# Optimization experiments

Hardware: AMD Instinct MI355X
Metric: run time of the kernel (lower is better)

The kernel has to match this reference:

```python
import jax, jax.numpy as jnp
import numpy as np

B, D_IN, D_EXP, D_TOW, N_EXP, N_TASK = 16384, 1024, 1024, 512, 8, 4


def setup_inputs() -> dict:
    key = jax.random.key(0)
    ks = jax.random.split(key, 8)
    s_in = 1.0 / np.sqrt(D_IN)
    s_exp = 1.0 / np.sqrt(D_EXP)
    s_tow = 1.0 / np.sqrt(D_TOW)
    return {
        "x": jax.random.normal(ks[0], (B, D_IN), jnp.float32),
        # gate: ParameterList of num_experts vectors of size input_size -> [D_IN, N_EXP] matrix
        "gate_w": jax.random.normal(ks[1], (D_IN, N_EXP), jnp.float32) * s_in,
        # per-expert SLP: Linear(input_size, expert_size) + ReLU
        "exp_w": jax.random.normal(ks[2], (N_EXP, D_IN, D_EXP), jnp.float32) * s_in,
        "exp_b": jax.random.normal(ks[3], (N_EXP, D_EXP), jnp.float32) * 0.01,
        # per-task tower MLP: Linear(expert_size, tower_size) + ReLU + Linear(tower_size, 1)
        "tw1": jax.random.normal(ks[4], (N_TASK, D_EXP, D_TOW), jnp.float32) * s_exp,
        "tb1": jax.random.normal(ks[5], (N_TASK, D_TOW), jnp.float32) * 0.01,
        "tw2": jax.random.normal(ks[6], (N_TASK, D_TOW, 1), jnp.float32) * s_tow,
        "tb2": jax.random.normal(ks[7], (N_TASK, 1), jnp.float32) * 0.01,
    }


def reference(x, gate_w, exp_w, exp_b, tw1, tb1, tw2, tb2):
    # gates = x @ gate (no softmax in original)        [B, E]
    gates = x @ gate_w
    # all experts in one batched GEMM                  [E, B, D_exp]
    h = jax.nn.relu(jnp.einsum("bi,eid->ebd", x, exp_w) + exp_b[:, None, :])
    # fused gate-weighted combine (replaces the nested Python loops)
    shared = jnp.einsum("be,ebd->bd", gates, h)        # [B, D_exp]
    # per-task towers, batched over tasks
    t = jax.nn.relu(jnp.einsum("bd,tdh->tbh", shared, tw1) + tb1[:, None, :])
    outs = jnp.einsum("tbh,tho->tbo", t, tw2) + tb2[:, None, :]  # [T, B, 1]
    return outs
```

## Files before the change

### kernel.cpp

```cpp
#include <hip/hip_runtime.h>
#include <hip/hip_bf16.h>

#define B_DIM   16384
#define D_IN    1024
#define D_EXP   1024
#define D_TOW   512
#define N_EXPT  8
#define N_TASK  4

typedef _Float16 f16x8 __attribute__((ext_vector_type(8)));
typedef _Float16 f16x4 __attribute__((ext_vector_type(4)));
typedef float    f32x4 __attribute__((ext_vector_type(4)));

__device__ __forceinline__ void gll16(const void* g, void* l) {
  __builtin_amdgcn_global_load_lds(
      (const __attribute__((address_space(1))) unsigned int*)g,
      (__attribute__((address_space(3))) unsigned int*)l,
      16, 0, 0);
}

__device__ __forceinline__ f16x8 ldfrag(const _Float16* sM, int rowbase, int ks, int lane) {
  int rl = rowbase + (lane & 15);
  int ch = ((ks << 2) + (lane >> 4)) ^ (rl & 7);
  return *(const f16x8*)&sM[rl * 64 + ch * 8];
}

__global__ __launch_bounds__(256) void prep_x_kernel(
    const float* __restrict__ x, const float* __restrict__ gw,
    _Float16* __restrict__ xh, float* __restrict__ gates)
{
  __shared__ float sred[4][8];
  const int t = threadIdx.x;
  const long row = blockIdx.x;
  float4 v = ((const float4*)(x + row * D_IN))[t];
  f16x4 h;
  h[0] = (_Float16)v.x; h[1] = (_Float16)v.y; h[2] = (_Float16)v.z; h[3] = (_Float16)v.w;
  ((f16x4*)(xh + row * D_IN))[t] = h;

  float g[8];
#pragma unroll
  for (int e = 0; e < 8; ++e) g[e] = 0.f;
  const float* wp = gw + (size_t)t * 4 * 8;
  float xs[4] = {v.x, v.y, v.z, v.w};
#pragma unroll
  for (int j = 0; j < 4; ++j)
#pragma unroll
    for (int e = 0; e < 8; ++e) g[e] += xs[j] * wp[j * 8 + e];

#pragma unroll
  for (int e = 0; e < 8; ++e) {
    g[e] += __shfl_xor(g[e], 1);  g[e] += __shfl_xor(g[e], 2);
    g[e] += __shfl_xor(g[e], 4);  g[e] += __shfl_xor(g[e], 8);
    g[e] += __shfl_xor(g[e], 16); g[e] += __shfl_xor(g[e], 32);
  }
  if ((t & 63) == 0) {
#pragma unroll
    for (int e = 0; e < 8; ++e) sred[t >> 6][e] = g[e];
  }
  __syncthreads();
  if (t < 8) gates[row * 8 + t] = sred[0][t] + sred[1][t] + sred[2][t] + sred[3][t];
}

__global__ __launch_bounds__(256) void transpose_cvt_kernel(
    const float* __restrict__ in, _Float16* __restrict__ outp, int K, int N)
{
  __shared__ float tile[64][65];
  const int t = threadIdx.x;
  const int tx = t & 63, ty = t >> 6;
  const int n0 = blockIdx.x * 64;
  const int k0 = blockIdx.y * 64;
  const long s = blockIdx.z;
  const float* ip = in + s * (long)K * N;
  _Float16* op = outp + s * (long)K * N;
#pragma unroll
  for (int i = 0; i < 16; ++i) {
    int r = ty * 16 + i;
    tile[r][tx] = ip[(long)(k0 + r) * N + n0 + tx];
  }
  __syncthreads();
#pragma unroll
  for (int i = 0; i < 16; ++i) {
    int r = ty * 16 + i;
    op[(long)(n0 + r) * K + k0 + tx] = (_Float16)tile[tx][r];
  }
}

__global__ void init_out_kernel(float* __restrict__ out, const float* __restrict__ tb2) {
  int i = blockIdx.x * 256 + threadIdx.x;
  if (i < N_TASK * B_DIM) out[i] = tb2[i >> 14];
}

#define PHASE(SLOT, H, STAGES, WAITS)                                          \
  do {                                                                         \
    const _Float16* sAq = &sT[SLOT][(wm >> 1) * 8192];                         \
    const _Float16* sBq = &sT[SLOT][16384 + wn * 4096];                        \
    f16x8 af[2][2];                                                            \
    _Pragma("unroll") for (int m2 = 0; m2 < 2; ++m2)                           \
      _Pragma("unroll") for (int ks = 0; ks < 2; ++ks)                         \
        af[m2][ks] = ldfrag(sAq, (wm & 1) * 64 + ((H) * 2 + m2) * 16, ks, lane);\
    if ((H) == 0) {                                                            \
      _Pragma("unroll") for (int nf = 0; nf < 4; ++nf)                         \
        _Pragma("unroll") for (int ks = 0; ks < 2; ++ks)                       \
          bf[nf][ks] = ldfrag(sBq, nf * 16, ks, lane);                         \
    }                                                                          \
    STAGES;                                                                    \
    asm volatile("" ::: "memory");                                             \
    __builtin_amdgcn_s_barrier();                                              \
    asm volatile("s_waitcnt lgkmcnt(0)" ::: "memory");                         \
    __builtin_amdgcn_sched_barrier(0);                                         \
    __builtin_amdgcn_s_setprio(1);                                             \
    _Pragma("unroll") for (int m2 = 0; m2 < 2; ++m2)                           \
      _Pragma("unroll") for (int nf = 0; nf < 4; ++nf)                         \
        _Pragma("unroll") for (int ks = 0; ks < 2; ++ks)                       \
          acc[(H) * 2 + m2][nf] = __builtin_amdgcn_mfma_f32_16x16x32_f16(      \
              af[m2][ks], bf[nf][ks], acc[(H) * 2 + m2][nf], 0, 0, 0);         \
    __builtin_amdgcn_s_setprio(0);                                             \
    WAITS;                                                                     \
    asm volatile("" ::: "memory");                                             \
    __builtin_amdgcn_s_barrier();                                              \
  } while (0)

__global__ __launch_bounds__(512, 2) void moe_expert_kernel(
    const _Float16* __restrict__ xh,
    const _Float16* __restrict__ ewT,
    const float* __restrict__ expb,
    const float* __restrict__ gates,
    _Float16* __restrict__ shout)
{
  __shared__ alignas(16) _Float16 sT[2][24576];
  __shared__ float sG[256 * 8];
  __shared__ float sBias[8 * 128];
  const int t = threadIdx.x;
  const int lane = t & 63;
  const int wave = t >> 6;
  const int wm = wave >> 1, wn = wave & 1;
  const long row0 = (long)blockIdx.x * 256;
  const int col0 = blockIdx.y * 128;

  for (int i = t; i < 256 * 8; i += 512) sG[i] = gates[row0 * 8 + i];
  for (int i = t; i < 8 * 128; i += 512)
    sBias[i] = expb[(i >> 7) * D_EXP + col0 + (i & 127)];

  const int so_t = (((t & 7) ^ ((t >> 3) & 7)) << 4);
  const char* aBase = (const char*)xh + row0 * 2048 + (size_t)(t >> 3) * 2048 + so_t;
  const char* bRoot = (const char*)ewT + (size_t)col0 * 2048 + (size_t)(t >> 3) * 2048 + so_t;

  auto SA = [&](int s, int h, int step) {
    const char* g = aBase + (size_t)h * 262144 + (size_t)(step & 15) * 128;
    char* d = (char*)&sT[s][h * 8192] + t * 16;
    gll16(g, d);
    gll16(g + 131072, d + 8192);
    asm volatile("" ::: "memory");
  };
  auto SB = [&](int s, int h, int step) {
    const char* g = bRoot + (size_t)(step >> 4) * 2097152 + (size_t)h * 131072
                    + (size_t)(step & 15) * 128;
    char* d = (char*)&sT[s][16384 + h * 4096] + t * 16;
    gll16(g, d);
    asm volatile("" ::: "memory");
  };

  __syncthreads();

  SB(0, 0, 0); SB(0, 1, 0);
  SA(0, 0, 0); SA(0, 1, 0);
  SB(1, 0, 1); SB(1, 1, 1);
  asm volatile("s_waitcnt vmcnt(2)" ::: "memory");
  __builtin_amdgcn_s_barrier();

  f32x4 acc[4][4] = {};
  f32x4 shacc[4][4] = {};
  f16x8 bf[4][2];

  for (int it = 0; it < 64; ++it) {
    const int kt1 = 2 * it + 1;
    const bool pf = (it < 63);

    PHASE(0, 0, { SA(1, 0, kt1); SA(1, 1, kt1); }, {});
    PHASE(0, 1, { if (pf) { SB(0, 0, 2 * it + 2); SB(0, 1, 2 * it + 2); } },
          { if (pf) { asm volatile("s_waitcnt vmcnt(2)" ::: "memory"); }
            else    { asm volatile("s_waitcnt vmcnt(0)" ::: "memory"); } });
    PHASE(1, 0, { if (pf) { SA(0, 0, 2 * it + 2); SA(0, 1, 2 * it + 2); } }, {});
    PHASE(1, 1, { if (pf) { SB(1, 0, 2 * it + 3); SB(1, 1, 2 * it + 3); } },
          { if (pf) { asm volatile("s_waitcnt vmcnt(2)" ::: "memory"); } });

    if ((it & 7) == 7) {
      const int e = it >> 3;
      float bias4[4];
#pragma unroll
      for (int nf = 0; nf < 4; ++nf)
        bias4[nf] = sBias[e * 128 + wn * 64 + nf * 16 + (lane & 15)];
#pragma unroll
      for (int mf = 0; mf < 4; ++mf) {
        int rbase = wm * 64 + mf * 16 + ((lane >> 4) << 2);
        float gv[4];
#pragma unroll
        for (int r = 0; r < 4; ++r) gv[r] = sG[(rbase + r) * 8 + e];
#pragma unroll
        for (int nf = 0; nf < 4; ++nf)
#pragma unroll
          for (int r = 0; r < 4; ++r) {
            float hv = acc[mf][nf][r] + bias4[nf];
            hv = hv > 0.f ? hv : 0.f;
            shacc[mf][nf][r] += gv[r] * hv;
            acc[mf][nf][r] = 0.f;
          }
      }
    }
  }

#pragma unroll
  for (int mf = 0; mf < 4; ++mf)
#pragma unroll
    for (int r = 0; r < 4; ++r) {
      long row = row0 + wm * 64 + mf * 16 + ((lane >> 4) << 2) + r;
      _Float16* op = shout + row * D_EXP + col0 + wn * 64 + (lane & 15);
#pragma unroll
      for (int nf = 0; nf < 4; ++nf) op[nf * 16] = (_Float16)shacc[mf][nf][r];
    }
}

__global__ __launch_bounds__(512, 2) void moe_tower_kernel(
    const _Float16* __restrict__ sh,
    const _Float16* __restrict__ t1T,
    const float* __restrict__ tb1,
    const float* __restrict__ tw2,
    float* __restrict__ out)
{
  __shared__ alignas(16) _Float16 sT[2][24576];
  const int t = threadIdx.x;
  const int lane = t & 63;
  const int wave = t >> 6;
  const int wm = wave >> 1, wn = wave & 1;
  const long row0 = (long)blockIdx.x * 256;
  const int task = blockIdx.y >> 2;
  const int col0 = (blockIdx.y & 3) * 128;

  float b1[4], w2[4];
#pragma unroll
  for (int nf = 0; nf < 4; ++nf) {
    int col = col0 + wn * 64 + nf * 16 + (lane & 15);
    b1[nf] = tb1[task * D_TOW + col];
    w2[nf] = tw2[task * D_TOW + col];
  }
  asm volatile("" ::: "memory");

  const int so_t = (((t & 7) ^ ((t >> 3) & 7)) << 4);
  const char* aBase = (const char*)sh + row0 * 2048 + (size_t)(t >> 3) * 2048 + so_t;
  const char* bRoot = (const char*)t1T + (size_t)task * (D_TOW * D_EXP * 2)
                      + (size_t)col0 * 2048 + (size_t)(t >> 3) * 2048 + so_t;

  auto SA = [&](int s, int h, int step) {
    const char* g = aBase + (size_t)h * 262144 + (size_t)step * 128;
    char* d = (char*)&sT[s][h * 8192] + t * 16;
    gll16(g, d);
    gll16(g + 131072, d + 8192);
    asm volatile("" ::: "memory");
  };
  auto SB = [&](int s, int h, int step) {
    const char* g = bRoot + (size_t)h * 131072 + (size_t)step * 128;
    char* d = (char*)&sT[s][16384 + h * 4096] + t * 16;
    gll16(g, d);
    asm volatile("" ::: "memory");
  };

  __syncthreads();

  SB(0, 0, 0); SB(0, 1, 0);
  SA(0, 0, 0); SA(0, 1, 0);
  SB(1, 0, 1); SB(1, 1, 1);
  asm volatile("s_waitcnt vmcnt(2)" ::: "memory");
  __builtin_amdgcn_s_barrier();

  f32x4 acc[4][4] = {};
  f16x8 bf[4][2];

  for (int it = 0; it < 8; ++it) {
    const int kt1 = 2 * it + 1;
    const bool pf = (it < 7);

    PHASE(0, 0, { SA(1, 0, kt1); SA(1, 1, kt1); }, {});
    PHASE(0, 1, { if (pf) { SB(0, 0, 2 * it + 2); SB(0, 1, 2 * it + 2); } },
          { if (pf) { asm volatile("s_waitcnt vmcnt(2)" ::: "memory"); }
            else    { asm volatile("s_waitcnt vmcnt(0)" ::: "memory"); } });
    PHASE(1, 0, { if (pf) { SA(0, 0, 2 * it + 2); SA(0, 1, 2 * it + 2); } }, {});
    PHASE(1, 1, { if (pf) { SB(1, 0, 2 * it + 3); SB(1, 1, 2 * it + 3); } },
          { if (pf) { asm volatile("s_waitcnt vmcnt(2)" ::: "memory"); } });
  }

#pragma unroll
  for (int mf = 0; mf < 4; ++mf)
#pragma unroll
    for (int r = 0; r < 4; ++r) {
      float ssum = 0.f;
#pragma unroll
      for (int nf = 0; nf < 4; ++nf) {
        float v = acc[mf][nf][r] + b1[nf];
        v = v > 0.f ? v : 0.f;
        ssum += v * w2[nf];
      }
      ssum += __shfl_xor(ssum, 1);
      ssum += __shfl_xor(ssum, 2);
      ssum += __shfl_xor(ssum, 4);
      ssum += __shfl_xor(ssum, 8);
      if ((lane & 15) == 0) {
        long row = row0 + wm * 64 + mf * 16 + ((lane >> 4) << 2) + r;
        atomicAdd(&out[(size_t)task * B_DIM + row], ssum);
      }
    }
}

extern "C" void kernel_launch(void* const* d_in, const int* in_sizes, int n_in,
                              void* d_out, int out_size, void* d_ws, size_t ws_size,
                              hipStream_t stream) {
  const float* x    = (const float*)d_in[0];
  const float* gw   = (const float*)d_in[1];
  const float* expw = (const float*)d_in[2];
  const float* expb = (const float*)d_in[3];
  const float* tw1  = (const float*)d_in[4];
  const float* tb1  = (const float*)d_in[5];
  const float* tw2  = (const float*)d_in[6];
  const float* tb2  = (const float*)d_in[7];
  float* out = (float*)d_out;

  char* ws = (char*)d_ws;
  _Float16* xh  = (_Float16*)ws;  ws += (size_t)B_DIM * D_IN * 2;
  _Float16* ewT = (_Float16*)ws;  ws += (size_t)N_EXPT * D_IN * D_EXP * 2;
  _Float16* t1T = (_Float16*)ws;  ws += (size_t)N_TASK * D_TOW * D_EXP * 2;
  _Float16* shh = (_Float16*)ws;  ws += (size_t)B_DIM * D_EXP * 2;
  float* gates  = (float*)ws;     ws += (size_t)B_DIM * N_EXPT * 4;

  prep_x_kernel<<<B_DIM, 256, 0, stream>>>(x, gw, xh, gates);
  transpose_cvt_kernel<<<dim3(D_EXP / 64, D_IN / 64, N_EXPT), 256, 0, stream>>>(
      expw, ewT, D_IN, D_EXP);
  transpose_cvt_kernel<<<dim3(D_TOW / 64, D_EXP / 64, N_TASK), 256, 0, stream>>>(
      tw1, t1T, D_EXP, D_TOW);
  init_out_kernel<<<(N_TASK * B_DIM + 255) / 256, 256, 0, stream>>>(out, tb2);
  moe_expert_kernel<<<dim3(B_DIM / 256, D_EXP / 128), 512, 0, stream>>>(
      xh, ewT, expb, gates, shh);
  moe_tower_kernel<<<dim3(B_DIM / 256, (N_TASK * D_TOW) / 128), 512, 0, stream>>>(
      shh, t1T, tb1, tw2, out);
}
```

Measured before the change: 420.1 us.

## Enlarge GEMM block tile to 256x256 with 2x4 wave grid and fp16 shared accumulators

Both the expert and tower GEMM kernels move from 256x128 to 256x256 block tiles. Waves are rearranged into a 2x4 grid, each computing 128x64, and every k-step is split into four staged phases with finer-grained prefetch and an extra lgkmcnt wait. The aim is to halve global A-tile traffic per output and raise MFMA work per LDS byte. In the expert kernel the gated accumulator shacc becomes fp16 to save registers, which costs precision. The larger tile doubles LDS (about 128KB+) and the accumulator registers, so occupancy at launch_bounds(512,2) is at risk and the grid gets fewer blocks.

```diff
diff --git a/kernel.cpp b/kernel.cpp
--- a/kernel.cpp
+++ b/kernel.cpp
@@ -90,21 +90,22 @@
   if (i < N_TASK * B_DIM) out[i] = tb2[i >> 14];
 }
 
-#define PHASE(SLOT, H, STAGES, WAITS)                                          \
+#define PH(SLOT, Q, STAGES, WAITS)                                             \
   do {                                                                         \
-    const _Float16* sAq = &sT[SLOT][(wm >> 1) * 8192];                         \
-    const _Float16* sBq = &sT[SLOT][16384 + wn * 4096];                        \
+    const _Float16* sAq = &sT[SLOT][wm * 8192];                                \
+    const _Float16* sBq = &sT[SLOT][16384 + (wn >> 1) * 8192];                 \
     f16x8 af[2][2];                                                            \
     _Pragma("unroll") for (int m2 = 0; m2 < 2; ++m2)                           \
       _Pragma("unroll") for (int ks = 0; ks < 2; ++ks)                         \
-        af[m2][ks] = ldfrag(sAq, (wm & 1) * 64 + ((H) * 2 + m2) * 16, ks, lane);\
-    if ((H) == 0) {                                                            \
+        af[m2][ks] = ldfrag(sAq, ((Q) * 2 + m2) * 16, ks, lane);               \
+    if ((Q) == 0) {                                                            \
       _Pragma("unroll") for (int nf = 0; nf < 4; ++nf)                         \
         _Pragma("unroll") for (int ks = 0; ks < 2; ++ks)                       \
-          bf[nf][ks] = ldfrag(sBq, nf * 16, ks, lane);                         \
+          bf[nf][ks] = ldfrag(sBq, (wn & 1) * 64 + nf * 16, ks, lane);         \
     }                                                                          \
     STAGES;                                                                    \
     asm volatile("" ::: "memory");                                             \
+    if ((Q) == 0) { asm volatile("s_waitcnt lgkmcnt(8)" ::: "memory"); }       \
     __builtin_amdgcn_s_barrier();                                              \
     asm volatile("s_waitcnt lgkmcnt(0)" ::: "memory");                         \
     __builtin_amdgcn_sched_barrier(0);                                         \
@@ -112,8 +113,8 @@
     _Pragma("unroll") for (int m2 = 0; m2 < 2; ++m2)                           \
       _Pragma("unroll") for (int nf = 0; nf < 4; ++nf)                         \
         _Pragma("unroll") for (int ks = 0; ks < 2; ++ks)                       \
-          acc[(H) * 2 + m2][nf] = __builtin_amdgcn_mfma_f32_16x16x32_f16(      \
-              af[m2][ks], bf[nf][ks], acc[(H) * 2 + m2][nf], 0, 0, 0);         \
+          acc[(Q) * 2 + m2][nf] = __builtin_amdgcn_mfma_f32_16x16x32_f16(      \
+              af[m2][ks], bf[nf][ks], acc[(Q) * 2 + m2][nf], 0, 0, 0);         \
     __builtin_amdgcn_s_setprio(0);                                             \
     WAITS;                                                                     \
     asm volatile("" ::: "memory");                                             \
@@ -127,36 +128,36 @@
     const float* __restrict__ gates,
     _Float16* __restrict__ shout)
 {
-  __shared__ alignas(16) _Float16 sT[2][24576];
+  __shared__ alignas(16) _Float16 sT[2][32768];
   __shared__ float sG[256 * 8];
-  __shared__ float sBias[8 * 128];
+  __shared__ float sBias[8 * 256];
   const int t = threadIdx.x;
   const int lane = t & 63;
   const int wave = t >> 6;
-  const int wm = wave >> 1, wn = wave & 1;
+  const int wm = wave >> 2, wn = wave & 3;
   const long row0 = (long)blockIdx.x * 256;
-  const int col0 = blockIdx.y * 128;
+  const int col0 = blockIdx.y * 256;
 
   for (int i = t; i < 256 * 8; i += 512) sG[i] = gates[row0 * 8 + i];
-  for (int i = t; i < 8 * 128; i += 512)
-    sBias[i] = expb[(i >> 7) * D_EXP + col0 + (i & 127)];
+  for (int i = t; i < 8 * 256; i += 512)
+    sBias[i] = expb[(i >> 8) * D_EXP + col0 + (i & 255)];
 
   const int so_t = (((t & 7) ^ ((t >> 3) & 7)) << 4);
   const char* aBase = (const char*)xh + row0 * 2048 + (size_t)(t >> 3) * 2048 + so_t;
   const char* bRoot = (const char*)ewT + (size_t)col0 * 2048 + (size_t)(t >> 3) * 2048 + so_t;
-
-  auto SA = [&](int s, int h, int step) {
-    const char* g = aBase + (size_t)h * 262144 + (size_t)(step & 15) * 128;
-    char* d = (char*)&sT[s][h * 8192] + t * 16;
-    gll16(g, d);
-    gll16(g + 131072, d + 8192);
+  char* sTB = (char*)&sT[0][0];
+
+  auto SA = [&](int s, int h, int kt) {
+    const char* g = aBase + (size_t)h * 262144 + (size_t)(kt & 15) * 128;
+    char* d = sTB + s * 65536 + h * 16384 + t * 16;
+    gll16(g, d); gll16(g + 131072, d + 8192);
     asm volatile("" ::: "memory");
   };
-  auto SB = [&](int s, int h, int step) {
-    const char* g = bRoot + (size_t)(step >> 4) * 2097152 + (size_t)h * 131072
-                    + (size_t)(step & 15) * 128;
-    char* d = (char*)&sT[s][16384 + h * 4096] + t * 16;
-    gll16(g, d);
+  auto SB = [&](int s, int h, int kt) {
+    const char* g = bRoot + (size_t)(kt >> 4) * 2097152 + (size_t)h * 262144
+                    + (size_t)(kt & 15) * 128;
+    char* d = sTB + s * 65536 + 32768 + h * 16384 + t * 16;
+    gll16(g, d); gll16(g + 131072, d + 8192);
     asm volatile("" ::: "memory");
   };
 
@@ -165,58 +166,65 @@
   SB(0, 0, 0); SB(0, 1, 0);
   SA(0, 0, 0); SA(0, 1, 0);
   SB(1, 0, 1); SB(1, 1, 1);
-  asm volatile("s_waitcnt vmcnt(2)" ::: "memory");
+  asm volatile("s_waitcnt vmcnt(4)" ::: "memory");
   __builtin_amdgcn_s_barrier();
 
-  f32x4 acc[4][4] = {};
-  f32x4 shacc[4][4] = {};
+  f32x4 acc[8][4] = {};
+  f16x4 shacc[8][4] = {};
   f16x8 bf[4][2];
 
   for (int it = 0; it < 64; ++it) {
-    const int kt1 = 2 * it + 1;
+    const int kt0 = 2 * it, kt1 = 2 * it + 1;
     const bool pf = (it < 63);
 
-    PHASE(0, 0, { SA(1, 0, kt1); SA(1, 1, kt1); }, {});
-    PHASE(0, 1, { if (pf) { SB(0, 0, 2 * it + 2); SB(0, 1, 2 * it + 2); } },
-          { if (pf) { asm volatile("s_waitcnt vmcnt(2)" ::: "memory"); }
-            else    { asm volatile("s_waitcnt vmcnt(0)" ::: "memory"); } });
-    PHASE(1, 0, { if (pf) { SA(0, 0, 2 * it + 2); SA(0, 1, 2 * it + 2); } }, {});
-    PHASE(1, 1, { if (pf) { SB(1, 0, 2 * it + 3); SB(1, 1, 2 * it + 3); } },
-          { if (pf) { asm volatile("s_waitcnt vmcnt(2)" ::: "memory"); } });
+    PH(0, 0, { SA(1, 0, kt1); }, {});
+    PH(0, 1, { SA(1, 1, kt1); }, {});
+    PH(0, 2, { if (pf) SB(0, 0, kt0 + 2); }, {});
+    PH(0, 3, { if (pf) SB(0, 1, kt0 + 2); },
+       { if (pf) { asm volatile("s_waitcnt vmcnt(4)" ::: "memory"); }
+         else    { asm volatile("s_waitcnt vmcnt(0)" ::: "memory"); } });
+    PH(1, 0, { if (pf) SA(0, 0, kt0 + 2); }, {});
+    PH(1, 1, { if (pf) SA(0, 1, kt0 + 2); }, {});
+    PH(1, 2, { if (pf) SB(1, 0, kt1 + 2); }, {});
+    PH(1, 3, { if (pf) SB(1, 1, kt1 + 2); },
+       { if (pf) { asm volatile("s_waitcnt vmcnt(4)" ::: "memory"); } });
 
     if ((it & 7) == 7) {
       const int e = it >> 3;
       float bias4[4];
 #pragma unroll
       for (int nf = 0; nf < 4; ++nf)
-        bias4[nf] = sBias[e * 128 + wn * 64 + nf * 16 + (lane & 15)];
-#pragma unroll
-      for (int mf = 0; mf < 4; ++mf) {
-        int rbase = wm * 64 + mf * 16 + ((lane >> 4) << 2);
+        bias4[nf] = sBias[e * 256 + wn * 64 + nf * 16 + (lane & 15)];
+#pragma unroll
+      for (int mf = 0; mf < 8; ++mf) {
+        int rbase = wm * 128 + mf * 16 + ((lane >> 4) << 2);
         float gv[4];
 #pragma unroll
         for (int r = 0; r < 4; ++r) gv[r] = sG[(rbase + r) * 8 + e];
 #pragma unroll
-        for (int nf = 0; nf < 4; ++nf)
+        for (int nf = 0; nf < 4; ++nf) {
+          f16x4 sh = shacc[mf][nf];
 #pragma unroll
           for (int r = 0; r < 4; ++r) {
             float hv = acc[mf][nf][r] + bias4[nf];
             hv = hv > 0.f ? hv : 0.f;
-            shacc[mf][nf][r] += gv[r] * hv;
-            acc[mf][nf][r] = 0.f;
+            sh[r] += (_Float16)(gv[r] * hv);
           }
+          shacc[mf][nf] = sh;
+          acc[mf][nf] = f32x4{0.f, 0.f, 0.f, 0.f};
+        }
       }
     }
   }
 
 #pragma unroll
-  for (int mf = 0; mf < 4; ++mf)
+  for (int mf = 0; mf < 8; ++mf)
 #pragma unroll
     for (int r = 0; r < 4; ++r) {
-      long row = row0 + wm * 64 + mf * 16 + ((lane >> 4) << 2) + r;
+      long row = row0 + wm * 128 + mf * 16 + ((lane >> 4) << 2) + r;
       _Float16* op = shout + row * D_EXP + col0 + wn * 64 + (lane & 15);
 #pragma unroll
-      for (int nf = 0; nf < 4; ++nf) op[nf * 16] = (_Float16)shacc[mf][nf][r];
+      for (int nf = 0; nf < 4; ++nf) op[nf * 16] = shacc[mf][nf][r];
     }
 }
 
@@ -227,14 +235,14 @@
     const float* __restrict__ tw2,
     float* __restrict__ out)
 {
-  __shared__ alignas(16) _Float16 sT[2][24576];
+  __shared__ alignas(16) _Float16 sT[2][32768];
   const int t = threadIdx.x;
   const int lane = t & 63;
   const int wave = t >> 6;
-  const int wm = wave >> 1, wn = wave & 1;
+  const int wm = wave >> 2, wn = wave & 3;
   const long row0 = (long)blockIdx.x * 256;
-  const int task = blockIdx.y >> 2;
-  const int col0 = (blockIdx.y & 3) * 128;
+  const int task = blockIdx.y >> 1;
+  const int col0 = (blockIdx.y & 1) * 256;
 
   float b1[4], w2[4];
 #pragma unroll
@@ -243,24 +251,24 @@
     b1[nf] = tb1[task * D_TOW + col];
     w2[nf] = tw2[task * D_TOW + col];
   }
-  asm volatile("" ::: "memory");
+  asm volatile("s_waitcnt vmcnt(0)" ::: "memory");
 
   const int so_t = (((t & 7) ^ ((t >> 3) & 7)) << 4);
   const char* aBase = (const char*)sh + row0 * 2048 + (size_t)(t >> 3) * 2048 + so_t;
   const char* bRoot = (const char*)t1T + (size_t)task * (D_TOW * D_EXP * 2)
                       + (size_t)col0 * 2048 + (size_t)(t >> 3) * 2048 + so_t;
-
-  auto SA = [&](int s, int h, int step) {
-    const char* g = aBase + (size_t)h * 262144 + (size_t)step * 128;
-    char* d = (char*)&sT[s][h * 8192] + t * 16;
-    gll16(g, d);
-    gll16(g + 131072, d + 8192);
+  char* sTB = (char*)&sT[0][0];
+
+  auto SA = [&](int s, int h, int kt) {
+    const char* g = aBase + (size_t)h * 262144 + (size_t)kt * 128;
+    char* d = sTB + s * 65536 + h * 16384 + t * 16;
+    gll16(g, d); gll16(g + 131072, d + 8192);
     asm volatile("" ::: "memory");
   };
-  auto SB = [&](int s, int h, int step) {
-    const char* g = bRoot + (size_t)h * 131072 + (size_t)step * 128;
-    char* d = (char*)&sT[s][16384 + h * 4096] + t * 16;
-    gll16(g, d);
+  auto SB = [&](int s, int h, int kt) {
+    const char* g = bRoot + (size_t)h * 262144 + (size_t)kt * 128;
+    char* d = sTB + s * 65536 + 32768 + h * 16384 + t * 16;
+    gll16(g, d); gll16(g + 131072, d + 8192);
     asm volatile("" ::: "memory");
   };
 
@@ -269,27 +277,31 @@
   SB(0, 0, 0); SB(0, 1, 0);
   SA(0, 0, 0); SA(0, 1, 0);
   SB(1, 0, 1); SB(1, 1, 1);
-  asm volatile("s_waitcnt vmcnt(2)" ::: "memory");
+  asm volatile("s_waitcnt vmcnt(4)" ::: "memory");
   __builtin_amdgcn_s_barrier();
 
-  f32x4 acc[4][4] = {};
+  f32x4 acc[8][4] = {};
   f16x8 bf[4][2];
 
   for (int it = 0; it < 8; ++it) {
-    const int kt1 = 2 * it + 1;
+    const int kt0 = 2 * it, kt1 = 2 * it + 1;
     const bool pf = (it < 7);
 
-    PHASE(0, 0, { SA(1, 0, kt1); SA(1, 1, kt1); }, {});
-    PHASE(0, 1, { if (pf) { SB(0, 0, 2 * it + 2); SB(0, 1, 2 * it + 2); } },
-          { if (pf) { asm volatile("s_waitcnt vmcnt(2)" ::: "memory"); }
-            else    { asm volatile("s_waitcnt vmcnt(0)" ::: "memory"); } });
-    PHASE(1, 0, { if (pf) { SA(0, 0, 2 * it + 2); SA(0, 1, 2 * it + 2); } }, {});
-    PHASE(1, 1, { if (pf) { SB(1, 0, 2 * it + 3); SB(1, 1, 2 * it + 3); } },
-          { if (pf) { asm volatile("s_waitcnt vmcnt(2)" ::: "memory"); } });
-  }
-
-#pragma unroll
-  for (int mf = 0; mf < 4; ++mf)
+    PH(0, 0, { SA(1, 0, kt1); }, {});
+    PH(0, 1, { SA(1, 1, kt1); }, {});
+    PH(0, 2, { if (pf) SB(0, 0, kt0 + 2); }, {});
+    PH(0, 3, { if (pf) SB(0, 1, kt0 + 2); },
+       { if (pf) { asm volatile("s_waitcnt vmcnt(4)" ::: "memory"); }
+         else    { asm volatile("s_waitcnt vmcnt(0)" ::: "memory"); } });
+    PH(1, 0, { if (pf) SA(0, 0, kt0 + 2); }, {});
+    PH(1, 1, { if (pf) SA(0, 1, kt0 + 2); }, {});
+    PH(1, 2, { if (pf) SB(1, 0, kt1 + 2); }, {});
+    PH(1, 3, { if (pf) SB(1, 1, kt1 + 2); },
+       { if (pf) { asm volatile("s_waitcnt vmcnt(4)" ::: "memory"); } });
+  }
+
+#pragma unroll
+  for (int mf = 0; mf < 8; ++mf)
 #pragma unroll
     for (int r = 0; r < 4; ++r) {
       float ssum = 0.f;
@@ -304,7 +316,7 @@
       ssum += __shfl_xor(ssum, 4);
       ssum += __shfl_xor(ssum, 8);
       if ((lane & 15) == 0) {
-        long row = row0 + wm * 64 + mf * 16 + ((lane >> 4) << 2) + r;
+        long row = row0 + wm * 128 + mf * 16 + ((lane >> 4) << 2) + r;
         atomicAdd(&out[(size_t)task * B_DIM + row], ssum);
       }
     }
@@ -336,8 +348,8 @@
   transpose_cvt_kernel<<<dim3(D_TOW / 64, D_EXP / 64, N_TASK), 256, 0, stream>>>(
       tw1, t1T, D_EXP, D_TOW);
   init_out_kernel<<<(N_TASK * B_DIM + 255) / 256, 256, 0, stream>>>(out, tb2);
-  moe_expert_kernel<<<dim3(B_DIM / 256, D_EXP / 128), 512, 0, stream>>>(
+  moe_expert_kernel<<<dim3(B_DIM / 256, D_EXP / 256), 512, 0, stream>>>(
       xh, ewT, expb, gates, shh);
-  moe_tower_kernel<<<dim3(B_DIM / 256, (N_TASK * D_TOW) / 128), 512, 0, stream>>>(
+  moe_tower_kernel<<<dim3(B_DIM / 256, N_TASK * (D_TOW / 256)), 512, 0, stream>>>(
       shh, t1T, tb1, tw2, out);
 }
```

After: 448.8 us. +6.8%, slower.

## Switch expert and tower GEMMs to 32x32x16 MFMA tiles

Applied to the files above, without the earlier changes.

Replaces the 16x16x32 MFMA instructions with 32x32x16 MFMA in both GEMM kernels. The fragment loads, accumulator layout, epilogue row mapping and LDS staging offsets change to match the larger tile shape, with fewer fragment loads per MFMA. The expert kernel's gated-sum accumulator also moves from fp32 to fp16 registers to cut register pressure, which loses precision in the accumulation over experts. The LDS staging offsets were rewritten (A halves at 16384-byte stride, B at 32768 + 8192*h) while the sT array size stayed the same, so the new layout may not line up with the old buffer.

```diff
diff --git a/kernel.cpp b/kernel.cpp
--- a/kernel.cpp
+++ b/kernel.cpp
@@ -10,7 +10,9 @@
 
 typedef _Float16 f16x8 __attribute__((ext_vector_type(8)));
 typedef _Float16 f16x4 __attribute__((ext_vector_type(4)));
+typedef _Float16 f16x16h __attribute__((ext_vector_type(16)));
 typedef float    f32x4 __attribute__((ext_vector_type(4)));
+typedef float    f32x16 __attribute__((ext_vector_type(16)));
 
 __device__ __forceinline__ void gll16(const void* g, void* l) {
   __builtin_amdgcn_global_load_lds(
@@ -19,9 +21,9 @@
       16, 0, 0);
 }
 
-__device__ __forceinline__ f16x8 ldfrag(const _Float16* sM, int rowbase, int ks, int lane) {
-  int rl = rowbase + (lane & 15);
-  int ch = ((ks << 2) + (lane >> 4)) ^ (rl & 7);
+__device__ __forceinline__ f16x8 ldfrag32(const _Float16* sM, int rowbase, int s, int lane) {
+  int rl = rowbase + (lane & 31);
+  int ch = ((s << 1) + (lane >> 5)) ^ (rl & 7);
   return *(const f16x8*)&sM[rl * 64 + ch * 8];
 }
 
@@ -90,18 +92,17 @@
   if (i < N_TASK * B_DIM) out[i] = tb2[i >> 14];
 }
 
-#define PHASE(SLOT, H, STAGES, WAITS)                                          \
+#define PHASE32(SLOT, H, STAGES, WAITS)                                        \
   do {                                                                         \
     const _Float16* sAq = &sT[SLOT][(wm >> 1) * 8192];                         \
     const _Float16* sBq = &sT[SLOT][16384 + wn * 4096];                        \
-    f16x8 af[2][2];                                                            \
-    _Pragma("unroll") for (int m2 = 0; m2 < 2; ++m2)                           \
-      _Pragma("unroll") for (int ks = 0; ks < 2; ++ks)                         \
-        af[m2][ks] = ldfrag(sAq, (wm & 1) * 64 + ((H) * 2 + m2) * 16, ks, lane);\
+    f16x8 af[4];                                                               \
+    _Pragma("unroll") for (int s = 0; s < 4; ++s)                              \
+      af[s] = ldfrag32(sAq, (wm & 1) * 64 + (H) * 32, s, lane);                \
     if ((H) == 0) {                                                            \
-      _Pragma("unroll") for (int nf = 0; nf < 4; ++nf)                         \
-        _Pragma("unroll") for (int ks = 0; ks < 2; ++ks)                       \
-          bf[nf][ks] = ldfrag(sBq, nf * 16, ks, lane);                         \
+      _Pragma("unroll") for (int nt = 0; nt < 2; ++nt)                         \
+        _Pragma("unroll") for (int s = 0; s < 4; ++s)                          \
+          bf[nt][s] = ldfrag32(sBq, nt * 32, s, lane);                         \
     }                                                                          \
     STAGES;                                                                    \
     asm volatile("" ::: "memory");                                             \
@@ -109,11 +110,10 @@
     asm volatile("s_waitcnt lgkmcnt(0)" ::: "memory");                         \
     __builtin_amdgcn_sched_barrier(0);                                         \
     __builtin_amdgcn_s_setprio(1);                                             \
-    _Pragma("unroll") for (int m2 = 0; m2 < 2; ++m2)                           \
-      _Pragma("unroll") for (int nf = 0; nf < 4; ++nf)                         \
-        _Pragma("unroll") for (int ks = 0; ks < 2; ++ks)                       \
-          acc[(H) * 2 + m2][nf] = __builtin_amdgcn_mfma_f32_16x16x32_f16(      \
-              af[m2][ks], bf[nf][ks], acc[(H) * 2 + m2][nf], 0, 0, 0);         \
+    _Pragma("unroll") for (int s = 0; s < 4; ++s)                              \
+      _Pragma("unroll") for (int nt = 0; nt < 2; ++nt)                         \
+        acc[H][nt] = __builtin_amdgcn_mfma_f32_32x32x16_f16(                   \
+            af[s], bf[nt][s], acc[H][nt], 0, 0, 0);                            \
     __builtin_amdgcn_s_setprio(0);                                             \
     WAITS;                                                                     \
     asm volatile("" ::: "memory");                                             \
@@ -147,7 +147,7 @@
 
   auto SA = [&](int s, int h, int step) {
     const char* g = aBase + (size_t)h * 262144 + (size_t)(step & 15) * 128;
-    char* d = (char*)&sT[s][h * 8192] + t * 16;
+    char* d = (char*)&sT[s][0] + h * 16384 + t * 16;
     gll16(g, d);
     gll16(g + 131072, d + 8192);
     asm volatile("" ::: "memory");
@@ -155,7 +155,7 @@
   auto SB = [&](int s, int h, int step) {
     const char* g = bRoot + (size_t)(step >> 4) * 2097152 + (size_t)h * 131072
                     + (size_t)(step & 15) * 128;
-    char* d = (char*)&sT[s][16384 + h * 4096] + t * 16;
+    char* d = (char*)&sT[s][0] + 32768 + h * 8192 + t * 16;
     gll16(g, d);
     asm volatile("" ::: "memory");
   };
@@ -168,56 +168,55 @@
   asm volatile("s_waitcnt vmcnt(2)" ::: "memory");
   __builtin_amdgcn_s_barrier();
 
-  f32x4 acc[4][4] = {};
-  f32x4 shacc[4][4] = {};
-  f16x8 bf[4][2];
+  f32x16 acc[2][2] = {};
+  f16x16h shacc[2][2] = {};
+  f16x8 bf[2][4];
 
   for (int it = 0; it < 64; ++it) {
     const int kt1 = 2 * it + 1;
     const bool pf = (it < 63);
 
-    PHASE(0, 0, { SA(1, 0, kt1); SA(1, 1, kt1); }, {});
-    PHASE(0, 1, { if (pf) { SB(0, 0, 2 * it + 2); SB(0, 1, 2 * it + 2); } },
+    PHASE32(0, 0, { SA(1, 0, kt1); SA(1, 1, kt1); }, {});
+    PHASE32(0, 1, { if (pf) { SB(0, 0, 2 * it + 2); SB(0, 1, 2 * it + 2); } },
           { if (pf) { asm volatile("s_waitcnt vmcnt(2)" ::: "memory"); }
             else    { asm volatile("s_waitcnt vmcnt(0)" ::: "memory"); } });
-    PHASE(1, 0, { if (pf) { SA(0, 0, 2 * it + 2); SA(0, 1, 2 * it + 2); } }, {});
-    PHASE(1, 1, { if (pf) { SB(1, 0, 2 * it + 3); SB(1, 1, 2 * it + 3); } },
+    PHASE32(1, 0, { if (pf) { SA(0, 0, 2 * it + 2); SA(0, 1, 2 * it + 2); } }, {});
+    PHASE32(1, 1, { if (pf) { SB(1, 0, 2 * it + 3); SB(1, 1, 2 * it + 3); } },
           { if (pf) { asm volatile("s_waitcnt vmcnt(2)" ::: "memory"); } });
 
     if ((it & 7) == 7) {
       const int e = it >> 3;
-      float bias4[4];
-#pragma unroll
-      for (int nf = 0; nf < 4; ++nf)
-        bias4[nf] = sBias[e * 128 + wn * 64 + nf * 16 + (lane & 15)];
-#pragma unroll
-      for (int mf = 0; mf < 4; ++mf) {
-        int rbase = wm * 64 + mf * 16 + ((lane >> 4) << 2);
-        float gv[4];
-#pragma unroll
-        for (int r = 0; r < 4; ++r) gv[r] = sG[(rbase + r) * 8 + e];
-#pragma unroll
-        for (int nf = 0; nf < 4; ++nf)
-#pragma unroll
-          for (int r = 0; r < 4; ++r) {
-            float hv = acc[mf][nf][r] + bias4[nf];
+#pragma unroll
+      for (int mt = 0; mt < 2; ++mt)
+#pragma unroll
+        for (int nt = 0; nt < 2; ++nt) {
+          float biasv = sBias[e * 128 + wn * 64 + nt * 32 + (lane & 31)];
+          f16x16h shv = shacc[mt][nt];
+#pragma unroll
+          for (int reg = 0; reg < 16; ++reg) {
+            int r = (reg & 3) + 8 * (reg >> 2) + 4 * (lane >> 5);
+            int rowl = wm * 64 + mt * 32 + r;
+            float gv = sG[rowl * 8 + e];
+            float hv = acc[mt][nt][reg] + biasv;
             hv = hv > 0.f ? hv : 0.f;
-            shacc[mf][nf][r] += gv[r] * hv;
-            acc[mf][nf][r] = 0.f;
+            shv[reg] += (_Float16)(gv * hv);
+            acc[mt][nt][reg] = 0.f;
           }
+          shacc[mt][nt] = shv;
+        }
+    }
+  }
+
+#pragma unroll
+  for (int mt = 0; mt < 2; ++mt)
+#pragma unroll
+    for (int nt = 0; nt < 2; ++nt)
+#pragma unroll
+      for (int reg = 0; reg < 16; ++reg) {
+        int r = (reg & 3) + 8 * (reg >> 2) + 4 * (lane >> 5);
+        long row = row0 + wm * 64 + mt * 32 + r;
+        shout[row * D_EXP + col0 + wn * 64 + nt * 32 + (lane & 31)] = shacc[mt][nt][reg];
       }
-    }
-  }
-
-#pragma unroll
-  for (int mf = 0; mf < 4; ++mf)
-#pragma unroll
-    for (int r = 0; r < 4; ++r) {
-      long row = row0 + wm * 64 + mf * 16 + ((lane >> 4) << 2) + r;
-      _Float16* op = shout + row * D_EXP + col0 + wn * 64 + (lane & 15);
-#pragma unroll
-      for (int nf = 0; nf < 4; ++nf) op[nf * 16] = (_Float16)shacc[mf][nf][r];
-    }
 }
 
 __global__ __launch_bounds__(512, 2) void moe_tower_kernel(
@@ -236,14 +235,14 @@
   const int task = blockIdx.y >> 2;
   const int col0 = (blockIdx.y & 3) * 128;
 
-  float b1[4], w2[4];
-#pragma unroll
-  for (int nf = 0; nf < 4; ++nf) {
-    int col = col0 + wn * 64 + nf * 16 + (lane & 15);
-    b1[nf] = tb1[task * D_TOW + col];
-    w2[nf] = tw2[task * D_TOW + col];
-  }
-  asm volatile("" ::: "memory");
+  float b1[2], w2[2];
+#pragma unroll
+  for (int nt = 0; nt < 2; ++nt) {
+    int col = col0 + wn * 64 + nt * 32 + (lane & 31);
+    b1[nt] = tb1[task * D_TOW + col];
+    w2[nt] = tw2[task * D_TOW + col];
+  }
+  asm volatile("s_waitcnt vmcnt(0)" ::: "memory");
 
   const int so_t = (((t & 7) ^ ((t >> 3) & 7)) << 4);
   const char* aBase = (const char*)sh + row0 * 2048 + (size_t)(t >> 3) * 2048 + so_t;
@@ -252,14 +251,14 @@
 
   auto SA = [&](int s, int h, int step) {
     const char* g = aBase + (size_t)h * 262144 + (size_t)step * 128;
-    char* d = (char*)&sT[s][h * 8192] + t * 16;
+    char* d = (char*)&sT[s][0] + h * 16384 + t * 16;
     gll16(g, d);
     gll16(g + 131072, d + 8192);
     asm volatile("" ::: "memory");
   };
   auto SB = [&](int s, int h, int step) {
     const char* g = bRoot + (size_t)h * 131072 + (size_t)step * 128;
-    char* d = (char*)&sT[s][16384 + h * 4096] + t * 16;
+    char* d = (char*)&sT[s][0] + 32768 + h * 8192 + t * 16;
     gll16(g, d);
     asm volatile("" ::: "memory");
   };
@@ -272,39 +271,41 @@
   asm volatile("s_waitcnt vmcnt(2)" ::: "memory");
   __builtin_amdgcn_s_barrier();
 
-  f32x4 acc[4][4] = {};
-  f16x8 bf[4][2];
+  f32x16 acc[2][2] = {};
+  f16x8 bf[2][4];
 
   for (int it = 0; it < 8; ++it) {
     const int kt1 = 2 * it + 1;
     const bool pf = (it < 7);
 
-    PHASE(0, 0, { SA(1, 0, kt1); SA(1, 1, kt1); }, {});
-    PHASE(0, 1, { if (pf) { SB(0, 0, 2 * it + 2); SB(0, 1, 2 * it + 2); } },
+    PHASE32(0, 0, { SA(1, 0, kt1); SA(1, 1, kt1); }, {});
+    PHASE32(0, 1, { if (pf) { SB(0, 0, 2 * it + 2); SB(0, 1, 2 * it + 2); } },
           { if (pf) { asm volatile("s_waitcnt vmcnt(2)" ::: "memory"); }
             else    { asm volatile("s_waitcnt vmcnt(0)" ::: "memory"); } });
-    PHASE(1, 0, { if (pf) { SA(0, 0, 2 * it + 2); SA(0, 1, 2 * it + 2); } }, {});
-    PHASE(1, 1, { if (pf) { SB(1, 0, 2 * it + 3); SB(1, 1, 2 * it + 3); } },
+    PHASE32(1, 0, { if (pf) { SA(0, 0, 2 * it + 2); SA(0, 1, 2 * it + 2); } }, {});
+    PHASE32(1, 1, { if (pf) { SB(1, 0, 2 * it + 3); SB(1, 1, 2 * it + 3); } },
           { if (pf) { asm volatile("s_waitcnt vmcnt(2)" ::: "memory"); } });
   }
 
 #pragma unroll
-  for (int mf = 0; mf < 4; ++mf)
-#pragma unroll
-    for (int r = 0; r < 4; ++r) {
+  for (int mt = 0; mt < 2; ++mt)
+#pragma unroll
+    for (int reg = 0; reg < 16; ++reg) {
       float ssum = 0.f;
 #pragma unroll
-      for (int nf = 0; nf < 4; ++nf) {
-        float v = acc[mf][nf][r] + b1[nf];
+      for (int nt = 0; nt < 2; ++nt) {
+        float v = acc[mt][nt][reg] + b1[nt];
         v = v > 0.f ? v : 0.f;
-        ssum += v * w2[nf];
+        ssum += v * w2[nt];
       }
       ssum += __shfl_xor(ssum, 1);
       ssum += __shfl_xor(ssum, 2);
       ssum += __shfl_xor(ssum, 4);
       ssum += __shfl_xor(ssum, 8);
-      if ((lane & 15) == 0) {
-        long row = row0 + wm * 64 + mf * 16 + ((lane >> 4) << 2) + r;
+      ssum += __shfl_xor(ssum, 16);
+      if ((lane & 31) == 0) {
+        int r = (reg & 3) + 8 * (reg >> 2) + 4 * (lane >> 5);
+        long row = row0 + wm * 64 + mt * 32 + r;
         atomicAdd(&out[(size_t)task * B_DIM + row], ssum);
       }
     }
```

New measurement: 481.2 us. 1.15x slower.

## Switch expert and tower GEMMs to triple-buffered LDS pipeline with two-step prefetch

Applied to the files above, without the earlier changes.

Both GEMM kernels move from a double-buffered LDS scheme, which interleaved A and B tile loads across four phases, to a three-slot rotating buffer. Each k-step's A and B tiles are issued two steps ahead, so global-to-LDS loads have more latency slack. LDS use rises from 96KB to 144KB per block, which with launch_bounds(512,2) may exceed the per-CU LDS budget and cut occupancy. The expert bias is also stored in LDS as fp16 to save space, at a small cost in precision.

```diff
diff --git a/kernel.cpp b/kernel.cpp
--- a/kernel.cpp
+++ b/kernel.cpp
@@ -90,10 +90,10 @@
   if (i < N_TASK * B_DIM) out[i] = tb2[i >> 14];
 }
 
-#define PHASE(SLOT, H, STAGES, WAITS)                                          \
+#define PHASE3(PA, H, STAGES, WAITS)                                           \
   do {                                                                         \
-    const _Float16* sAq = &sT[SLOT][(wm >> 1) * 8192];                         \
-    const _Float16* sBq = &sT[SLOT][16384 + wn * 4096];                        \
+    const _Float16* sAq = (const _Float16*)(PA) + (wm >> 1) * 8192;            \
+    const _Float16* sBq = (const _Float16*)(PA) + 16384 + wn * 4096;           \
     f16x8 af[2][2];                                                            \
     _Pragma("unroll") for (int m2 = 0; m2 < 2; ++m2)                           \
       _Pragma("unroll") for (int ks = 0; ks < 2; ++ks)                         \
@@ -127,9 +127,9 @@
     const float* __restrict__ gates,
     _Float16* __restrict__ shout)
 {
-  __shared__ alignas(16) _Float16 sT[2][24576];
+  __shared__ alignas(16) _Float16 sT3[3][24576];
   __shared__ float sG[256 * 8];
-  __shared__ float sBias[8 * 128];
+  __shared__ _Float16 sBiasH[8 * 128];
   const int t = threadIdx.x;
   const int lane = t & 63;
   const int wave = t >> 6;
@@ -139,57 +139,54 @@
 
   for (int i = t; i < 256 * 8; i += 512) sG[i] = gates[row0 * 8 + i];
   for (int i = t; i < 8 * 128; i += 512)
-    sBias[i] = expb[(i >> 7) * D_EXP + col0 + (i & 127)];
+    sBiasH[i] = (_Float16)expb[(i >> 7) * D_EXP + col0 + (i & 127)];
 
   const int so_t = (((t & 7) ^ ((t >> 3) & 7)) << 4);
   const char* aBase = (const char*)xh + row0 * 2048 + (size_t)(t >> 3) * 2048 + so_t;
   const char* bRoot = (const char*)ewT + (size_t)col0 * 2048 + (size_t)(t >> 3) * 2048 + so_t;
 
-  auto SA = [&](int s, int h, int step) {
+  auto SA = [&](char* pS, int h, int step) {
     const char* g = aBase + (size_t)h * 262144 + (size_t)(step & 15) * 128;
-    char* d = (char*)&sT[s][h * 8192] + t * 16;
+    char* d = pS + h * 16384 + t * 16;
     gll16(g, d);
     gll16(g + 131072, d + 8192);
     asm volatile("" ::: "memory");
   };
-  auto SB = [&](int s, int h, int step) {
+  auto SB = [&](char* pS, int h, int step) {
     const char* g = bRoot + (size_t)(step >> 4) * 2097152 + (size_t)h * 131072
                     + (size_t)(step & 15) * 128;
-    char* d = (char*)&sT[s][16384 + h * 4096] + t * 16;
+    char* d = pS + 32768 + h * 8192 + t * 16;
     gll16(g, d);
     asm volatile("" ::: "memory");
   };
 
   __syncthreads();
 
-  SB(0, 0, 0); SB(0, 1, 0);
-  SA(0, 0, 0); SA(0, 1, 0);
-  SB(1, 0, 1); SB(1, 1, 1);
-  asm volatile("s_waitcnt vmcnt(2)" ::: "memory");
+  char* pA = (char*)&sT3[0][0];
+  char* pB = (char*)&sT3[1][0];
+  char* pC = (char*)&sT3[2][0];
+
+  SA(pA, 0, 0); SB(pA, 0, 0); SA(pA, 1, 0); SB(pA, 1, 0);
+  SA(pB, 0, 1); SB(pB, 0, 1); SA(pB, 1, 1); SB(pB, 1, 1);
+  asm volatile("s_waitcnt vmcnt(6)" ::: "memory");
   __builtin_amdgcn_s_barrier();
 
   f32x4 acc[4][4] = {};
   f32x4 shacc[4][4] = {};
   f16x8 bf[4][2];
 
-  for (int it = 0; it < 64; ++it) {
-    const int kt1 = 2 * it + 1;
-    const bool pf = (it < 63);
-
-    PHASE(0, 0, { SA(1, 0, kt1); SA(1, 1, kt1); }, {});
-    PHASE(0, 1, { if (pf) { SB(0, 0, 2 * it + 2); SB(0, 1, 2 * it + 2); } },
-          { if (pf) { asm volatile("s_waitcnt vmcnt(2)" ::: "memory"); }
-            else    { asm volatile("s_waitcnt vmcnt(0)" ::: "memory"); } });
-    PHASE(1, 0, { if (pf) { SA(0, 0, 2 * it + 2); SA(0, 1, 2 * it + 2); } }, {});
-    PHASE(1, 1, { if (pf) { SB(1, 0, 2 * it + 3); SB(1, 1, 2 * it + 3); } },
-          { if (pf) { asm volatile("s_waitcnt vmcnt(2)" ::: "memory"); } });
-
-    if ((it & 7) == 7) {
-      const int e = it >> 3;
+  for (int kt = 0; kt < 128; ++kt) {
+    PHASE3(pA, 0, { if (kt < 126) { SA(pC, 0, kt + 2); SB(pC, 0, kt + 2); } }, {});
+    PHASE3(pA, 1, { if (kt < 126) { SA(pC, 1, kt + 2); SB(pC, 1, kt + 2); } },
+        { if (kt < 126)      { asm volatile("s_waitcnt vmcnt(6)" ::: "memory"); }
+          else if (kt == 126){ asm volatile("s_waitcnt vmcnt(0)" ::: "memory"); } });
+
+    if ((kt & 15) == 15) {
+      const int e = kt >> 4;
       float bias4[4];
 #pragma unroll
       for (int nf = 0; nf < 4; ++nf)
-        bias4[nf] = sBias[e * 128 + wn * 64 + nf * 16 + (lane & 15)];
+        bias4[nf] = (float)sBiasH[e * 128 + wn * 64 + nf * 16 + (lane & 15)];
 #pragma unroll
       for (int mf = 0; mf < 4; ++mf) {
         int rbase = wm * 64 + mf * 16 + ((lane >> 4) << 2);
@@ -207,6 +204,8 @@
           }
       }
     }
+
+    char* tmp = pA; pA = pB; pB = pC; pC = tmp;
   }
 
 #pragma unroll
@@ -227,7 +226,7 @@
     const float* __restrict__ tw2,
     float* __restrict__ out)
 {
-  __shared__ alignas(16) _Float16 sT[2][24576];
+  __shared__ alignas(16) _Float16 sT3[3][24576];
   const int t = threadIdx.x;
   const int lane = t & 63;
   const int wave = t >> 6;
@@ -243,49 +242,48 @@
     b1[nf] = tb1[task * D_TOW + col];
     w2[nf] = tw2[task * D_TOW + col];
   }
-  asm volatile("" ::: "memory");
+  asm volatile("s_waitcnt vmcnt(0)" ::: "memory");
 
   const int so_t = (((t & 7) ^ ((t >> 3) & 7)) << 4);
   const char* aBase = (const char*)sh + row0 * 2048 + (size_t)(t >> 3) * 2048 + so_t;
   const char* bRoot = (const char*)t1T + (size_t)task * (D_TOW * D_EXP * 2)
                       + (size_t)col0 * 2048 + (size_t)(t >> 3) * 2048 + so_t;
 
-  auto SA = [&](int s, int h, int step) {
+  auto SA = [&](char* pS, int h, int step) {
     const char* g = aBase + (size_t)h * 262144 + (size_t)step * 128;
-    char* d = (char*)&sT[s][h * 8192] + t * 16;
+    char* d = pS + h * 16384 + t * 16;
     gll16(g, d);
     gll16(g + 131072, d + 8192);
     asm volatile("" ::: "memory");
   };
-  auto SB = [&](int s, int h, int step) {
+  auto SB = [&](char* pS, int h, int step) {
     const char* g = bRoot + (size_t)h * 131072 + (size_t)step * 128;
-    char* d = (char*)&sT[s][16384 + h * 4096] + t * 16;
+    char* d = pS + 32768 + h * 8192 + t * 16;
     gll16(g, d);
     asm volatile("" ::: "memory");
   };
 
   __syncthreads();
 
-  SB(0, 0, 0); SB(0, 1, 0);
-  SA(0, 0, 0); SA(0, 1, 0);
-  SB(1, 0, 1); SB(1, 1, 1);
-  asm volatile("s_waitcnt vmcnt(2)" ::: "memory");
+  char* pA = (char*)&sT3[0][0];
+  char* pB = (char*)&sT3[1][0];
+  char* pC = (char*)&sT3[2][0];
+
+  SA(pA, 0, 0); SB(pA, 0, 0); SA(pA, 1, 0); SB(pA, 1, 0);
+  SA(pB, 0, 1); SB(pB, 0, 1); SA(pB, 1, 1); SB(pB, 1, 1);
+  asm volatile("s_waitcnt vmcnt(6)" ::: "memory");
   __builtin_amdgcn_s_barrier();
 
   f32x4 acc[4][4] = {};
   f16x8 bf[4][2];
 
-  for (int it = 0; it < 8; ++it) {
-    const int kt1 = 2 * it + 1;
-    const bool pf = (it < 7);
-
-    PHASE(0, 0, { SA(1, 0, kt1); SA(1, 1, kt1); }, {});
-    PHASE(0, 1, { if (pf) { SB(0, 0, 2 * it + 2); SB(0, 1, 2 * it + 2); } },
-          { if (pf) { asm volatile("s_waitcnt vmcnt(2)" ::: "memory"); }
-            else    { asm volatile("s_waitcnt vmcnt(0)" ::: "memory"); } });
-    PHASE(1, 0, { if (pf) { SA(0, 0, 2 * it + 2); SA(0, 1, 2 * it + 2); } }, {});
-    PHASE(1, 1, { if (pf) { SB(1, 0, 2 * it + 3); SB(1, 1, 2 * it + 3); } },
-          { if (pf) { asm volatile("s_waitcnt vmcnt(2)" ::: "memory"); } });
+  for (int kt = 0; kt < 16; ++kt) {
+    PHASE3(pA, 0, { if (kt < 14) { SA(pC, 0, kt + 2); SB(pC, 0, kt + 2); } }, {});
+    PHASE3(pA, 1, { if (kt < 14) { SA(pC, 1, kt + 2); SB(pC, 1, kt + 2); } },
+        { if (kt < 14)       { asm volatile("s_waitcnt vmcnt(6)" ::: "memory"); }
+          else if (kt == 14) { asm volatile("s_waitcnt vmcnt(0)" ::: "memory"); } });
+
+    char* tmp = pA; pA = pB; pB = pC; pC = tmp;
   }
 
 #pragma unroll
```

Result: slower. 438.7 us (+4.4%).
